# Kernel tuning notes

Hardware: AMD Instinct MI355X
Metric: run time of the kernel (lower is better)

The kernel has to match this reference:

```python
import jax, jax.numpy as jnp
import numpy as np

B, S, D, H = 4, 1024, 1024, 16
DK = D // H


def _linear_params(key, scale):
    kw, kb = jax.random.split(key)
    W = jax.random.normal(kw, (D, D), dtype=jnp.float32) * scale
    b = jax.random.normal(kb, (D,), dtype=jnp.float32) * 0.01
    return W, b


def setup_inputs() -> dict:
    key = jax.random.key(0)
    ks = jax.random.split(key, 12)
    scale = 1.0 / np.sqrt(D)
    inp = {
        "query": jax.random.normal(ks[0], (B, S, D), dtype=jnp.float32),
        "key": jax.random.normal(ks[1], (B, S, D), dtype=jnp.float32),
        "value": jax.random.normal(ks[2], (B, S, D), dtype=jnp.float32),
        "time_k": jax.random.normal(ks[3], (B, S, D), dtype=jnp.float32),
        "time_v": jax.random.normal(ks[4], (B, S, D), dtype=jnp.float32),
        "mask": jnp.zeros((B, 1, S, S), dtype=jnp.float32),
    }
    names = ["Wq", "bq", "Wk", "bk", "Wv", "bv", "Wtk", "btk", "Wtv", "btv", "Wm", "bm"]
    for i in range(6):
        W, b = _linear_params(ks[5 + i], scale)
        inp[names[2 * i]] = W
        inp[names[2 * i + 1]] = b
    return inp


def _split_heads(x):
    # [B,S,D] -> [B,H,S,DK]
    b, s, _ = x.shape
    return x.reshape(b, s, H, DK).transpose(0, 2, 1, 3)


def reference(query, key, value, time_k, time_v, mask,
              Wq, bq, Wk, bk, Wv, bv, Wtk, btk, Wtv, btv, Wm, bm):
    q = _split_heads(query @ Wq + bq)
    k = _split_heads(key @ Wk + bk)
    v = _split_heads(value @ Wv + bv)
    t_k = _split_heads(time_k @ Wtk + btk)
    t_v = _split_heads(time_v @ Wtv + btv)

    # scores[b,h,i,j] = q_i . k_j + t_k_i . q_j  (note second term uses q on the key axis)
    scores = jnp.einsum("bhid,bhjd->bhij", q, k) + jnp.einsum("bhid,bhjd->bhij", t_k, q)
    # module divides by sqrt(d_model) (query.size(-1)), not sqrt(d_k)
    scores = scores / jnp.sqrt(jnp.float32(D)) + mask
    probs = jax.nn.softmax(scores, axis=-1)

    # dropout is identity (p=0 / eval); squeeze(-2) is a no-op for S>1
    context = jnp.einsum("bhij,bhjd->bhid", probs, v) + jnp.einsum("bhij,bhjd->bhid", probs, t_v)
    x = context.transpose(0, 2, 1, 3).reshape(query.shape[0], -1, D)
    return x @ Wm + bm
```

## Files before the change

kernel.cpp:

```cpp
#include <hip/hip_runtime.h>
#include <hip/hip_bf16.h>
#include <cstdint>
#include <cstddef>

typedef __bf16 bf16;
typedef bf16 bf16x8 __attribute__((ext_vector_type(8)));
typedef bf16 bf16x4 __attribute__((ext_vector_type(4)));
typedef float f32x4 __attribute__((ext_vector_type(4)));
typedef unsigned int u32;

#define DEV static __device__ __forceinline__

DEV f32x4 mfma16(bf16x8 a, bf16x8 b, f32x4 c) {
    return __builtin_amdgcn_mfma_f32_16x16x32_bf16(a, b, c, 0, 0, 0);
}

DEV f32x4 shflx4(f32x4 v, int m) {
    f32x4 r;
    for (int i = 0; i < 4; ++i) r[i] = __shfl_xor(v[i], m, 64);
    return r;
}

DEV bf16x8 cvt8(const float* p) {
    float4 f0 = *(const float4*)p;
    float4 f1 = *(const float4*)(p + 4);
    bf16x8 v;
    v[0] = (bf16)f0.x; v[1] = (bf16)f0.y; v[2] = (bf16)f0.z; v[3] = (bf16)f0.w;
    v[4] = (bf16)f1.x; v[5] = (bf16)f1.y; v[6] = (bf16)f1.z; v[7] = (bf16)f1.w;
    return v;
}

DEV void glo(const bf16* g, bf16* l) {
    __builtin_amdgcn_global_load_lds(
        (const __attribute__((address_space(1))) u32*)g,
        (__attribute__((address_space(3))) u32*)l,
        16, 0, 0);
}


struct PrepArgs {
    const float* w[6];
    const float* act[5];
    bf16* wt;
    bf16* actbf[5];
};

__global__ __launch_bounds__(256) void prep_kernel(PrepArgs p)
{
    const int z = blockIdx.z;
    const int t = threadIdx.x;
    if (z < 6) {
        __shared__ bf16 tile[64][72];
        const float* src = p.w[z];
        bf16* out = p.wt + (size_t)z * 1024 * 1024;
        const int r = t >> 3, c8 = (t & 7) * 8;
        const int row0 = blockIdx.y * 64, col0 = blockIdx.x * 64;
        *(bf16x8*)&tile[r][c8]      = cvt8(&src[(size_t)(row0 + r) * 1024 + col0 + c8]);
        *(bf16x8*)&tile[r + 32][c8] = cvt8(&src[(size_t)(row0 + r + 32) * 1024 + col0 + c8]);
        __syncthreads();
        for (int half = 0; half < 2; ++half) {
            int rr = r + half * 32;
            bf16x8 v;
            for (int j = 0; j < 8; ++j) v[j] = tile[c8 + j][rr];
            *(bf16x8*)&out[(size_t)(col0 + rr) * 1024 + row0 + c8] = v;
        }
    } else {
        const float* src = p.act[z - 6];
        bf16* dst = p.actbf[z - 6];
        const size_t chunk = (size_t)(blockIdx.y * 16 + blockIdx.x) * 16384;
        for (int c = 0; c < 8; ++c) {
            const size_t off = chunk + (size_t)c * 2048 + (size_t)t * 8;
            *(bf16x8*)&dst[off] = cvt8(&src[off]);
        }
    }
}

__global__ __launch_bounds__(256) void maskprep_kernel(
    const float* __restrict__ mask, bf16* __restrict__ maskR)
{
    const int jt = blockIdx.x, it = blockIdx.y, b = blockIdx.z;
    __shared__ bf16 Mt[128 * 72];
    const int t = threadIdx.x, lane = t & 63, w = t >> 6;
    const int ln = lane & 15, qd = lane >> 4;
    {
        const int il = t >> 1, jh = (t & 1) * 32;
        const float* src = &mask[((size_t)b * 1024 + it * 128 + il) * 1024 + jt * 64 + jh];
        *(bf16x8*)&Mt[il * 72 + jh]      = cvt8(src);
        *(bf16x8*)&Mt[il * 72 + jh + 8]  = cvt8(src + 8);
        *(bf16x8*)&Mt[il * 72 + jh + 16] = cvt8(src + 16);
        *(bf16x8*)&Mt[il * 72 + jh + 24] = cvt8(src + 24);
    }
    __syncthreads();
    bf16 m[32];
    for (int si = 0; si < 2; ++si)
        for (int jc = 0; jc < 4; ++jc)
            for (int r = 0; r < 4; ++r) {
                const int il = w * 32 + si * 16 + qd * 4 + r;
                const int jl = jc * 16 + ln;
                m[(si * 4 + jc) * 4 + r] = Mt[il * 72 + jl];
            }
    bf16* dst = &maskR[((((size_t)b * 8 + it) * 16 + jt) * 256 + t) * 32];
    for (int c = 0; c < 4; ++c)
        *(bf16x8*)&dst[c * 8] = *(const bf16x8*)&m[c * 8];
}

struct ProjArgs {
    const bf16* A[5];
    const bf16* W[5];
    const float* bias[5];
    bf16* out[5];
    int vst[5];
};

__global__ __launch_bounds__(256) void proj_gemm(ProjArgs pa)
{
    const int z = blockIdx.z;
    const bf16* A = pa.A[z];
    const bf16* W = pa.W[z];
    const int m0 = blockIdx.y * 128, n0 = blockIdx.x * 128;
    __shared__ bf16 As[128 * 64];
    __shared__ bf16 Bs[128 * 64];
    const int t = threadIdx.x, lane = t & 63, w = t >> 6;
    const int ln = lane & 15, qd = lane >> 4;
    const int wm0 = (w >> 1) * 64, wn0 = (w & 1) * 64;
    const int sub0 = w * 4;
    const int rr = lane >> 3;
    const int cbs = (((lane & 7) ^ rr)) * 8;
    const int lx = ln & 7;
    f32x4 acc[4][4];
    for (int i = 0; i < 4; ++i)
        for (int j = 0; j < 4; ++j)
            acc[i][j] = (f32x4){0.f, 0.f, 0.f, 0.f};
    for (int ks = 0; ks < 16; ++ks) {
        const int bk = ks * 64;
        __syncthreads();
        for (int i = 0; i < 4; ++i) {
            const int row = (sub0 + i) * 8 + rr;
            glo(&W[(size_t)(n0 + row) * 1024 + bk + cbs], &Bs[(sub0 + i) * 512]);
            glo(&A[(size_t)(m0 + row) * 1024 + bk + cbs], &As[(sub0 + i) * 512]);
        }
        __syncthreads();
        for (int kc = 0; kc < 2; ++kc) {
            const int sg = ((kc * 4 + qd) ^ lx) * 8;
            bf16x8 af[4], bfr[4];
            for (int mi = 0; mi < 4; ++mi)
                af[mi] = *(const bf16x8*)&As[(wm0 + mi * 16 + ln) * 64 + sg];
            for (int ni = 0; ni < 4; ++ni)
                bfr[ni] = *(const bf16x8*)&Bs[(wn0 + ni * 16 + ln) * 64 + sg];
            for (int mi = 0; mi < 4; ++mi)
                for (int ni = 0; ni < 4; ++ni)
                    acc[mi][ni] = mfma16(af[mi], bfr[ni], acc[mi][ni]);
        }
    }
    const float* bias = pa.bias[z];
    bf16* out = pa.out[z];
    const int vst = pa.vst[z];
    for (int ni = 0; ni < 4; ++ni) {
        const int n = n0 + wn0 + ni * 16 + ln;
        const float bv = bias[n];
        for (int mi = 0; mi < 4; ++mi) {
            const int mbase = m0 + wm0 + mi * 16 + qd * 4;
            f32x4 v = acc[mi][ni];
            if (vst) {
                const int b = mbase >> 10, s = mbase & 1023;
                bf16x4 pk;
                for (int r = 0; r < 4; ++r) pk[r] = (bf16)(v[r] + bv);
                *(bf16x4*)&out[((size_t)(b * 1024 + n)) * 1024 + s] = pk;
            } else {
                for (int r = 0; r < 4; ++r)
                    out[(size_t)(mbase + r) * 1024 + n] = (bf16)(v[r] + bv);
            }
        }
    }
}

__global__ __launch_bounds__(256) void attn6_kernel(
    const bf16* __restrict__ Qb, const bf16* __restrict__ Kb, const bf16* __restrict__ TKb,
    const bf16* __restrict__ Va, const bf16* __restrict__ Vb,
    const bf16* __restrict__ maskR, bf16* __restrict__ ctx)
{
    const int h = blockIdx.x, it = blockIdx.y, b = blockIdx.z;
    const int i0 = it * 128;
    __shared__ bf16 Ks[64 * 64];
    __shared__ bf16 QJs[64 * 64];
    __shared__ bf16 Vs[64 * 68];
    __shared__ bf16 Ps[128][68];
    const int t = threadIdx.x, lane = t & 63, w = t >> 6;
    const int ln = lane & 15, qd = lane >> 4;
    const int lx = ln & 7;
    const size_t baseQ = ((size_t)b * 1024) * 1024 + (size_t)h * 64;

    bf16x8 qf[2][2], tkf[2][2];
    for (int si = 0; si < 2; ++si) {
        const size_t row = (size_t)(i0 + w * 32 + si * 16 + ln);
        for (int kc = 0; kc < 2; ++kc) {
            qf[si][kc]  = *(const bf16x8*)&Qb [baseQ + row * 1024 + kc * 32 + qd * 8];
            tkf[si][kc] = *(const bf16x8*)&TKb[baseQ + row * 1024 + kc * 32 + qd * 8];
        }
    }

    f32x4 O[2][4];
    f32x4 psum[2];
    for (int si = 0; si < 2; ++si) {
        psum[si] = (f32x4){0.f, 0.f, 0.f, 0.f};
        for (int dc = 0; dc < 4; ++dc) O[si][dc] = (f32x4){0.f, 0.f, 0.f, 0.f};
    }

    const float c1 = 0.045084439f;
    const float c2 = 1.442695041f;

    const size_t mtile0 = (((size_t)b * 8 + it) * 16) * 256 + t;

    for (int jt = 0; jt < 16; ++jt) {
        const int j0 = jt * 64;
        __syncthreads();
        {
            const int rr = lane >> 3;
            const int cbs = ((lane & 7) ^ rr) * 8;
            for (int i = 0; i < 4; ++i) {
                const int u = w * 4 + i;
                if (u < 8) {
                    glo(&Kb[baseQ + (size_t)(j0 + u * 8 + rr) * 1024 + cbs], &Ks[u * 512]);
                } else {
                    const int s = u - 8;
                    glo(&Qb[baseQ + (size_t)(j0 + s * 8 + rr) * 1024 + cbs], &QJs[s * 512]);
                }
            }
        }
        {
            const int vrow = t >> 2, vcol = (t & 3) * 16;
            const size_t va = ((size_t)b * 1024 + h * 64 + vrow) * 1024 + j0 + vcol;
            bf16x8 a0 = *(const bf16x8*)&Va[va];
            bf16x8 a1 = *(const bf16x8*)&Va[va + 8];
            bf16x8 b0 = *(const bf16x8*)&Vb[va];
            bf16x8 b1 = *(const bf16x8*)&Vb[va + 8];
            bf16 s[16];
            for (int e = 0; e < 8; ++e) {
                s[e]     = (bf16)((float)a0[e] + (float)b0[e]);
                s[8 + e] = (bf16)((float)a1[e] + (float)b1[e]);
            }
            bf16* dst = &Vs[vrow * 68 + vcol];
            for (int c = 0; c < 4; ++c)
                *(bf16x4*)&dst[c * 4] = *(const bf16x4*)&s[c * 4];
        }
        bf16x8 mm[4];
        {
            const bf16* mb = &maskR[(mtile0 + (size_t)jt * 256) * 32];
            for (int c = 0; c < 4; ++c) mm[c] = *(const bf16x8*)&mb[c * 8];
        }
        __syncthreads();

        f32x4 sc[2][4];
        for (int jc = 0; jc < 4; ++jc) {
            bf16x8 kf[2], qjf[2];
            for (int kc = 0; kc < 2; ++kc) {
                const int sg = ((kc * 4 + qd) ^ lx) * 8;
                kf[kc]  = *(const bf16x8*)&Ks [(jc * 16 + ln) * 64 + sg];
                qjf[kc] = *(const bf16x8*)&QJs[(jc * 16 + ln) * 64 + sg];
            }
            for (int si = 0; si < 2; ++si) {
                f32x4 a = (f32x4){0.f, 0.f, 0.f, 0.f};
                a = mfma16(qf[si][0], kf[0], a);
                a = mfma16(qf[si][1], kf[1], a);
                a = mfma16(tkf[si][0], qjf[0], a);
                a = mfma16(tkf[si][1], qjf[1], a);
                sc[si][jc] = a;
            }
        }
        for (int si = 0; si < 2; ++si) {
            const int ibl = w * 32 + si * 16 + qd * 4;
            for (int jc = 0; jc < 4; ++jc) {
                const int jl = jc * 16 + ln;
                const int e = si * 4 + jc;
                for (int r = 0; r < 4; ++r) {
                    const float mval = (float)mm[e >> 1][(e & 1) * 4 + r];
                    const float p = exp2f(fmaf(sc[si][jc][r], c1, mval * c2));
                    psum[si][r] += p;
                    Ps[ibl + r][jl] = (bf16)p;
                }
            }
        }
        for (int kc = 0; kc < 2; ++kc) {
            bf16x8 pa[2], vb[4];
            for (int si = 0; si < 2; ++si) {
                bf16x4 lo = *(const bf16x4*)&Ps[w * 32 + si * 16 + ln][kc * 32 + qd * 8];
                bf16x4 hi = *(const bf16x4*)&Ps[w * 32 + si * 16 + ln][kc * 32 + qd * 8 + 4];
                for (int e = 0; e < 4; ++e) { pa[si][e] = lo[e]; pa[si][4 + e] = hi[e]; }
            }
            for (int dc = 0; dc < 4; ++dc) {
                bf16x4 lo = *(const bf16x4*)&Vs[(dc * 16 + ln) * 68 + kc * 32 + qd * 8];
                bf16x4 hi = *(const bf16x4*)&Vs[(dc * 16 + ln) * 68 + kc * 32 + qd * 8 + 4];
                for (int e = 0; e < 4; ++e) { vb[dc][e] = lo[e]; vb[dc][4 + e] = hi[e]; }
            }
            for (int si = 0; si < 2; ++si)
                for (int dc = 0; dc < 4; ++dc)
                    O[si][dc] = mfma16(pa[si], vb[dc], O[si][dc]);
        }
    }

    for (int si = 0; si < 2; ++si) {
        for (int m = 1; m <= 8; m <<= 1) psum[si] += shflx4(psum[si], m);
        f32x4 rl;
        for (int r = 0; r < 4; ++r) rl[r] = 1.0f / psum[si][r];
        const int ibase = i0 + w * 32 + si * 16 + qd * 4;
        for (int dc = 0; dc < 4; ++dc) {
            const int d = h * 64 + dc * 16 + ln;
            f32x4 v = O[si][dc] * rl;
            for (int r = 0; r < 4; ++r)
                ctx[((size_t)b * 1024 + ibase + r) * 1024 + d] = (bf16)v[r];
        }
    }
}

__global__ __launch_bounds__(256) void out_gemm(
    const bf16* __restrict__ A, const bf16* __restrict__ W,
    const float* __restrict__ bias, float* __restrict__ out)
{
    const int n0 = blockIdx.x * 128, m0 = blockIdx.y * 64;
    __shared__ bf16 As[64 * 64];
    __shared__ bf16 Bs[128 * 64];
    const int t = threadIdx.x, lane = t & 63, w = t >> 6;
    const int ln = lane & 15, qd = lane >> 4;
    const int wn0 = w * 32;
    const int rr = lane >> 3;
    const int cbs = ((lane & 7) ^ rr) * 8;
    const int lx = ln & 7;
    f32x4 acc[4][2];
    for (int i = 0; i < 4; ++i)
        for (int j = 0; j < 2; ++j)
            acc[i][j] = (f32x4){0.f, 0.f, 0.f, 0.f};
    for (int ks = 0; ks < 16; ++ks) {
        const int bk = ks * 64;
        __syncthreads();
        for (int i = 0; i < 6; ++i) {
            const int u = w * 6 + i;
            if (u < 8) {
                glo(&A[(size_t)(m0 + u * 8 + rr) * 1024 + bk + cbs], &As[u * 512]);
            } else {
                const int sub = u - 8;
                glo(&W[(size_t)(n0 + sub * 8 + rr) * 1024 + bk + cbs], &Bs[sub * 512]);
            }
        }
        __syncthreads();
        for (int kc = 0; kc < 2; ++kc) {
            const int sg = ((kc * 4 + qd) ^ lx) * 8;
            bf16x8 af[4], bfr[2];
            for (int mi = 0; mi < 4; ++mi)
                af[mi] = *(const bf16x8*)&As[(mi * 16 + ln) * 64 + sg];
            for (int ni = 0; ni < 2; ++ni)
                bfr[ni] = *(const bf16x8*)&Bs[(wn0 + ni * 16 + ln) * 64 + sg];
            for (int mi = 0; mi < 4; ++mi)
                for (int ni = 0; ni < 2; ++ni)
                    acc[mi][ni] = mfma16(af[mi], bfr[ni], acc[mi][ni]);
        }
    }
    for (int ni = 0; ni < 2; ++ni) {
        const int n = n0 + wn0 + ni * 16 + ln;
        const float bv = bias[n];
        for (int mi = 0; mi < 4; ++mi) {
            const int mbase = m0 + mi * 16 + qd * 4;
            f32x4 v = acc[mi][ni];
            for (int r = 0; r < 4; ++r)
                out[(size_t)(mbase + r) * 1024 + n] = v[r] + bv;
        }
    }
}

extern "C" void kernel_launch(void* const* d_in, const int* in_sizes, int n_in,
                              void* d_out, int out_size, void* d_ws, size_t ws_size,
                              hipStream_t stream)
{
    (void)in_sizes; (void)n_in; (void)out_size; (void)ws_size;
    const float* query  = (const float*)d_in[0];
    const float* key    = (const float*)d_in[1];
    const float* value  = (const float*)d_in[2];
    const float* time_k = (const float*)d_in[3];
    const float* time_v = (const float*)d_in[4];
    const float* mask   = (const float*)d_in[5];
    const float* Wq  = (const float*)d_in[6];  const float* bq  = (const float*)d_in[7];
    const float* Wk  = (const float*)d_in[8];  const float* bk  = (const float*)d_in[9];
    const float* Wv  = (const float*)d_in[10]; const float* bv  = (const float*)d_in[11];
    const float* Wtk = (const float*)d_in[12]; const float* btk = (const float*)d_in[13];
    const float* Wtv = (const float*)d_in[14]; const float* btv = (const float*)d_in[15];
    const float* Wm  = (const float*)d_in[16]; const float* bm  = (const float*)d_in[17];

    bf16* ws = (bf16*)d_ws;
    const size_t MM = (size_t)1024 * 1024;
    bf16* WT    = ws;
    bf16* qbf   = ws + 6 * MM;
    bf16* kbf   = ws + 10 * MM;
    bf16* vbf   = ws + 14 * MM;
    bf16* tkbf  = ws + 18 * MM;
    bf16* tvbf  = ws + 22 * MM;
    bf16* Qb    = ws + 26 * MM;
    bf16* Kb    = ws + 30 * MM;
    bf16* TKb   = ws + 34 * MM;
    bf16* VsTa  = ws + 38 * MM;
    bf16* VsTb  = ws + 42 * MM;
    bf16* ctx   = ws + 6 * MM;
    bf16* maskR = (bf16*)d_out;

    PrepArgs pp;
    pp.w[0] = Wq; pp.w[1] = Wk; pp.w[2] = Wv; pp.w[3] = Wtk; pp.w[4] = Wtv; pp.w[5] = Wm;
    pp.wt = WT;
    pp.act[0] = query; pp.act[1] = key; pp.act[2] = value;
    pp.act[3] = time_k; pp.act[4] = time_v;
    pp.actbf[0] = qbf; pp.actbf[1] = kbf; pp.actbf[2] = vbf;
    pp.actbf[3] = tkbf; pp.actbf[4] = tvbf;
    prep_kernel<<<dim3(16, 16, 11), 256, 0, stream>>>(pp);
    maskprep_kernel<<<dim3(16, 8, 4), 256, 0, stream>>>(mask, maskR);

    ProjArgs pa;
    pa.A[0] = qbf;  pa.W[0] = WT + 0 * MM; pa.bias[0] = bq;  pa.out[0] = Qb;   pa.vst[0] = 0;
    pa.A[1] = kbf;  pa.W[1] = WT + 1 * MM; pa.bias[1] = bk;  pa.out[1] = Kb;   pa.vst[1] = 0;
    pa.A[2] = tkbf; pa.W[2] = WT + 3 * MM; pa.bias[2] = btk; pa.out[2] = TKb;  pa.vst[2] = 0;
    pa.A[3] = vbf;  pa.W[3] = WT + 2 * MM; pa.bias[3] = bv;  pa.out[3] = VsTa; pa.vst[3] = 1;
    pa.A[4] = tvbf; pa.W[4] = WT + 4 * MM; pa.bias[4] = btv; pa.out[4] = VsTb; pa.vst[4] = 1;
    proj_gemm<<<dim3(8, 32, 5), 256, 0, stream>>>(pa);

    attn6_kernel<<<dim3(16, 8, 4), 256, 0, stream>>>(
        Qb, Kb, TKb, VsTa, VsTb, maskR, ctx);
    out_gemm<<<dim3(8, 64), 256, 0, stream>>>(ctx, WT + 5 * MM, bm, (float*)d_out);
}
```

Measured before the change: 326.9 us.

## Fuse fp32-to-bf16 activation conversion into projection GEMM loads

The separate pass that converted the five fp32 activation tensors to bf16 is removed. The projection GEMM now streams fp32 activation tiles straight into LDS with a swizzled layout and converts them to bf16 when building MFMA fragments. The grid order of the projection and output GEMMs is also swapped so consecutive blocks walk along M and share the same weight tile. This saves a full write and re-read of the activations, but doubles LDS use and global read volume for the A operand and adds conversion work inside the inner loop.

```diff
diff --git a/kernel.cpp b/kernel.cpp
--- a/kernel.cpp
+++ b/kernel.cpp
@@ -36,42 +36,36 @@
         (__attribute__((address_space(3))) u32*)l,
         16, 0, 0);
 }
+DEV void glof(const float* g, float* l) {
+    __builtin_amdgcn_global_load_lds(
+        (const __attribute__((address_space(1))) u32*)g,
+        (__attribute__((address_space(3))) u32*)l,
+        16, 0, 0);
+}
 
 
 struct PrepArgs {
     const float* w[6];
-    const float* act[5];
     bf16* wt;
-    bf16* actbf[5];
 };
 
 __global__ __launch_bounds__(256) void prep_kernel(PrepArgs p)
 {
     const int z = blockIdx.z;
     const int t = threadIdx.x;
-    if (z < 6) {
-        __shared__ bf16 tile[64][72];
-        const float* src = p.w[z];
-        bf16* out = p.wt + (size_t)z * 1024 * 1024;
-        const int r = t >> 3, c8 = (t & 7) * 8;
-        const int row0 = blockIdx.y * 64, col0 = blockIdx.x * 64;
-        *(bf16x8*)&tile[r][c8]      = cvt8(&src[(size_t)(row0 + r) * 1024 + col0 + c8]);
-        *(bf16x8*)&tile[r + 32][c8] = cvt8(&src[(size_t)(row0 + r + 32) * 1024 + col0 + c8]);
-        __syncthreads();
-        for (int half = 0; half < 2; ++half) {
-            int rr = r + half * 32;
-            bf16x8 v;
-            for (int j = 0; j < 8; ++j) v[j] = tile[c8 + j][rr];
-            *(bf16x8*)&out[(size_t)(col0 + rr) * 1024 + row0 + c8] = v;
-        }
-    } else {
-        const float* src = p.act[z - 6];
-        bf16* dst = p.actbf[z - 6];
-        const size_t chunk = (size_t)(blockIdx.y * 16 + blockIdx.x) * 16384;
-        for (int c = 0; c < 8; ++c) {
-            const size_t off = chunk + (size_t)c * 2048 + (size_t)t * 8;
-            *(bf16x8*)&dst[off] = cvt8(&src[off]);
-        }
+    __shared__ bf16 tile[64][72];
+    const float* src = p.w[z];
+    bf16* out = p.wt + (size_t)z * 1024 * 1024;
+    const int r = t >> 3, c8 = (t & 7) * 8;
+    const int row0 = blockIdx.y * 64, col0 = blockIdx.x * 64;
+    *(bf16x8*)&tile[r][c8]      = cvt8(&src[(size_t)(row0 + r) * 1024 + col0 + c8]);
+    *(bf16x8*)&tile[r + 32][c8] = cvt8(&src[(size_t)(row0 + r + 32) * 1024 + col0 + c8]);
+    __syncthreads();
+    for (int half = 0; half < 2; ++half) {
+        int rr = r + half * 32;
+        bf16x8 v;
+        for (int j = 0; j < 8; ++j) v[j] = tile[c8 + j][rr];
+        *(bf16x8*)&out[(size_t)(col0 + rr) * 1024 + row0 + c8] = v;
     }
 }
 
@@ -105,8 +99,8 @@
 }
 
 struct ProjArgs {
-    const bf16* A[5];
-    const bf16* W[5];
+    const float* A[5];
+    const bf16*  W[5];
     const float* bias[5];
     bf16* out[5];
     int vst[5];
@@ -115,18 +109,20 @@
 __global__ __launch_bounds__(256) void proj_gemm(ProjArgs pa)
 {
     const int z = blockIdx.z;
-    const bf16* A = pa.A[z];
-    const bf16* W = pa.W[z];
-    const int m0 = blockIdx.y * 128, n0 = blockIdx.x * 128;
-    __shared__ bf16 As[128 * 64];
-    __shared__ bf16 Bs[128 * 64];
+    const float* A = pa.A[z];
+    const bf16*  W = pa.W[z];
+    const int m0 = blockIdx.x * 128, n0 = blockIdx.y * 128;
+    __shared__ float Asf[128 * 64];
+    __shared__ bf16  Bs[128 * 64];
     const int t = threadIdx.x, lane = t & 63, w = t >> 6;
     const int ln = lane & 15, qd = lane >> 4;
     const int wm0 = (w >> 1) * 64, wn0 = (w & 1) * 64;
-    const int sub0 = w * 4;
-    const int rr = lane >> 3;
-    const int cbs = (((lane & 7) ^ rr)) * 8;
     const int lx = ln & 7;
+    const int brr = lane >> 3;
+    const int bcbs = ((lane & 7) ^ brr) * 8;
+    const int arr = lane >> 4;
+    const int c16 = lane & 15;
+    const int aseg = c16 >> 1, ahalf = c16 & 1;
     f32x4 acc[4][4];
     for (int i = 0; i < 4; ++i)
         for (int j = 0; j < 4; ++j)
@@ -134,19 +130,25 @@
     for (int ks = 0; ks < 16; ++ks) {
         const int bk = ks * 64;
         __syncthreads();
-        for (int i = 0; i < 4; ++i) {
-            const int row = (sub0 + i) * 8 + rr;
-            glo(&W[(size_t)(n0 + row) * 1024 + bk + cbs], &Bs[(sub0 + i) * 512]);
-            glo(&A[(size_t)(m0 + row) * 1024 + bk + cbs], &As[(sub0 + i) * 512]);
+        for (int j = 0; j < 4; ++j) {
+            const int u = w * 4 + j;
+            glo(&W[(size_t)(n0 + u * 8 + brr) * 1024 + bk + bcbs], &Bs[u * 512]);
+        }
+        for (int i = 0; i < 8; ++i) {
+            const int u = w * 8 + i;
+            const int row = u * 4 + arr;
+            const int colf = ((aseg ^ (row & 7)) * 8) + ahalf * 4;
+            glof(&A[(size_t)(m0 + row) * 1024 + bk + colf], &Asf[u * 256]);
         }
         __syncthreads();
         for (int kc = 0; kc < 2; ++kc) {
-            const int sg = ((kc * 4 + qd) ^ lx) * 8;
+            const int ksg = kc * 4 + qd;
+            const int sg = (ksg ^ lx);
             bf16x8 af[4], bfr[4];
             for (int mi = 0; mi < 4; ++mi)
-                af[mi] = *(const bf16x8*)&As[(wm0 + mi * 16 + ln) * 64 + sg];
+                af[mi] = cvt8(&Asf[(wm0 + mi * 16 + ln) * 64 + sg * 8]);
             for (int ni = 0; ni < 4; ++ni)
-                bfr[ni] = *(const bf16x8*)&Bs[(wn0 + ni * 16 + ln) * 64 + sg];
+                bfr[ni] = *(const bf16x8*)&Bs[(wn0 + ni * 16 + ln) * 64 + sg * 8];
             for (int mi = 0; mi < 4; ++mi)
                 for (int ni = 0; ni < 4; ++ni)
                     acc[mi][ni] = mfma16(af[mi], bfr[ni], acc[mi][ni]);
@@ -316,7 +318,7 @@
     const bf16* __restrict__ A, const bf16* __restrict__ W,
     const float* __restrict__ bias, float* __restrict__ out)
 {
-    const int n0 = blockIdx.x * 128, m0 = blockIdx.y * 64;
+    const int m0 = blockIdx.x * 64, n0 = blockIdx.y * 128;
     __shared__ bf16 As[64 * 64];
     __shared__ bf16 Bs[128 * 64];
     const int t = threadIdx.x, lane = t & 63, w = t >> 6;
@@ -387,38 +389,29 @@
     bf16* ws = (bf16*)d_ws;
     const size_t MM = (size_t)1024 * 1024;
     bf16* WT    = ws;
-    bf16* qbf   = ws + 6 * MM;
-    bf16* kbf   = ws + 10 * MM;
-    bf16* vbf   = ws + 14 * MM;
-    bf16* tkbf  = ws + 18 * MM;
-    bf16* tvbf  = ws + 22 * MM;
-    bf16* Qb    = ws + 26 * MM;
-    bf16* Kb    = ws + 30 * MM;
-    bf16* TKb   = ws + 34 * MM;
-    bf16* VsTa  = ws + 38 * MM;
-    bf16* VsTb  = ws + 42 * MM;
-    bf16* ctx   = ws + 6 * MM;
+    bf16* Qb    = ws + 6 * MM;
+    bf16* Kb    = ws + 10 * MM;
+    bf16* TKb   = ws + 14 * MM;
+    bf16* VsTa  = ws + 18 * MM;
+    bf16* VsTb  = ws + 22 * MM;
+    bf16* ctx   = ws + 26 * MM;
     bf16* maskR = (bf16*)d_out;
 
     PrepArgs pp;
     pp.w[0] = Wq; pp.w[1] = Wk; pp.w[2] = Wv; pp.w[3] = Wtk; pp.w[4] = Wtv; pp.w[5] = Wm;
     pp.wt = WT;
-    pp.act[0] = query; pp.act[1] = key; pp.act[2] = value;
-    pp.act[3] = time_k; pp.act[4] = time_v;
-    pp.actbf[0] = qbf; pp.actbf[1] = kbf; pp.actbf[2] = vbf;
-    pp.actbf[3] = tkbf; pp.actbf[4] = tvbf;
-    prep_kernel<<<dim3(16, 16, 11), 256, 0, stream>>>(pp);
+    prep_kernel<<<dim3(16, 16, 6), 256, 0, stream>>>(pp);
     maskprep_kernel<<<dim3(16, 8, 4), 256, 0, stream>>>(mask, maskR);
 
     ProjArgs pa;
-    pa.A[0] = qbf;  pa.W[0] = WT + 0 * MM; pa.bias[0] = bq;  pa.out[0] = Qb;   pa.vst[0] = 0;
-    pa.A[1] = kbf;  pa.W[1] = WT + 1 * MM; pa.bias[1] = bk;  pa.out[1] = Kb;   pa.vst[1] = 0;
-    pa.A[2] = tkbf; pa.W[2] = WT + 3 * MM; pa.bias[2] = btk; pa.out[2] = TKb;  pa.vst[2] = 0;
-    pa.A[3] = vbf;  pa.W[3] = WT + 2 * MM; pa.bias[3] = bv;  pa.out[3] = VsTa; pa.vst[3] = 1;
-    pa.A[4] = tvbf; pa.W[4] = WT + 4 * MM; pa.bias[4] = btv; pa.out[4] = VsTb; pa.vst[4] = 1;
-    proj_gemm<<<dim3(8, 32, 5), 256, 0, stream>>>(pa);
+    pa.A[0] = query;  pa.W[0] = WT + 0 * MM; pa.bias[0] = bq;  pa.out[0] = Qb;   pa.vst[0] = 0;
+    pa.A[1] = key;    pa.W[1] = WT + 1 * MM; pa.bias[1] = bk;  pa.out[1] = Kb;   pa.vst[1] = 0;
+    pa.A[2] = time_k; pa.W[2] = WT + 3 * MM; pa.bias[2] = btk; pa.out[2] = TKb;  pa.vst[2] = 0;
+    pa.A[3] = value;  pa.W[3] = WT + 2 * MM; pa.bias[3] = bv;  pa.out[3] = VsTa; pa.vst[3] = 1;
+    pa.A[4] = time_v; pa.W[4] = WT + 4 * MM; pa.bias[4] = btv; pa.out[4] = VsTb; pa.vst[4] = 1;
+    proj_gemm<<<dim3(32, 8, 5), 256, 0, stream>>>(pa);
 
     attn6_kernel<<<dim3(16, 8, 4), 256, 0, stream>>>(
         Qb, Kb, TKb, VsTa, VsTb, maskR, ctx);
-    out_gemm<<<dim3(8, 64), 256, 0, stream>>>(ctx, WT + 5 * MM, bm, (float*)d_out);
-}
+    out_gemm<<<dim3(64, 8), 256, 0, stream>>>(ctx, WT + 5 * MM, bm, (float*)d_out);
+}
```

Result: slower. 389.6 us (+19.2%).
